# Optimization experiments

Hardware: AMD Instinct MI355X
Metric: run time of the kernel (lower is better)

Reference implementation:

```python
import jax, jax.numpy as jnp
import numpy as np

B, N, HID = 8, 1024, 768
HEADS, LORA, HDIM = 12, 256, 64


def setup_inputs() -> dict:
    key = jax.random.key(0)
    k1, k2, k3 = jax.random.split(key, 3)
    hidden_states = jax.random.normal(k1, (B, N, HID), dtype=jnp.float32)
    attention_mask = jnp.ones((B, N), dtype=jnp.int32)
    # torch Linear weights are [out_features, in_features]
    Wt = jax.random.normal(k2, (HEADS, LORA, HID), dtype=jnp.float32) * (HID ** -0.5)
    Wa = jax.random.normal(k3, (HEADS, HDIM, LORA), dtype=jnp.float32) * (LORA ** -0.5)
    return {"hidden_states": hidden_states, "attention_mask": attention_mask,
            "Wt": Wt, "Wa": Wa}


def reference(hidden_states, attention_mask, Wt, Wa):
    # Per-head LoRA projection, batched over heads instead of a Python loop.
    # t: [b, h, n, head_dim]; repeat(1,1,3) in the original makes q = k = v = t.
    scale = hidden_states.shape[-1] ** -0.5  # input_dim ** -0.5
    t = jnp.einsum('bnd,hld->bhnl', hidden_states, Wt)
    t = jnp.einsum('bhnl,hel->bhne', t, Wa)
    scores = jnp.einsum('bhid,bhjd->bhij', t, t) * scale
    scores = jnp.where(attention_mask[:, None, None, :] == 0, -jnp.inf, scores)
    attn = jax.nn.softmax(scores, axis=-1)
    out = jnp.einsum('bhij,bhjd->bhid', attn, t)  # [b, h, n, d]
    b, h, n, d = out.shape
    return out.transpose(0, 2, 1, 3).reshape(b, n, h * d)
```

## Files before the change

### kernel.cpp

```cpp
#include <hip/hip_runtime.h>
#include <math.h>

#define BATCH 8
#define SEQ   1024
#define HID_  768
#define HEADS 12
#define LORA  256
#define HDIM  64

#define SCALE      0.03608439182435161f
#define SCALE_LOG2 0.05205863235888918f

typedef _Float16 f16_t;
typedef _Float16 f16x4 __attribute__((ext_vector_type(4)));
typedef _Float16 f16x8 __attribute__((ext_vector_type(8)));
typedef float    f32x4 __attribute__((ext_vector_type(4)));
typedef unsigned short ushort_t;

#define GLD16(g, l) __builtin_amdgcn_global_load_lds( \
    (const __attribute__((address_space(1))) void*)(g), \
    (__attribute__((address_space(3))) void*)(l), 16, 0, 0)

#define SW(c, r) ((((c) ^ ((r) & 7)) << 3))

#define N4_HS (BATCH * SEQ * HID_ / 4)
#define N4_WT (HEADS * LORA * HID_ / 4)
#define N4_WA (HEADS * HDIM * LORA / 4)

__global__ __launch_bounds__(256) void cvt_all_kernel(
    const float4* __restrict__ hs, const float4* __restrict__ wt,
    const float4* __restrict__ wa, f16x4* __restrict__ hs_f,
    f16x4* __restrict__ wt_f, f16x4* __restrict__ wa_f)
{
    int stride = gridDim.x * blockDim.x;
    for (int i = blockIdx.x * blockDim.x + threadIdx.x;
         i < N4_HS + N4_WT + N4_WA; i += stride) {
        const float4* s; f16x4* d; int j;
        if (i < N4_HS)                { s = hs; d = hs_f; j = i; }
        else if (i < N4_HS + N4_WT)   { s = wt; d = wt_f; j = i - N4_HS; }
        else                          { s = wa; d = wa_f; j = i - N4_HS - N4_WT; }
        float4 v = s[j];
        f16x4 o = {(f16_t)v.x, (f16_t)v.y, (f16_t)v.z, (f16_t)v.w};
        d[j] = o;
    }
}

__global__ __launch_bounds__(256, 3) void proj_mfma(
    const f16_t* __restrict__ hs_f, const f16_t* __restrict__ wt_f,
    const f16_t* __restrict__ wa_f, f16_t* __restrict__ t_f,
    f16_t* __restrict__ tT_f)
{
    __shared__ __attribute__((aligned(16))) char smem[32768];
    f16_t* s_hs = (f16_t*)smem;
    f16_t* s_wt = (f16_t*)(smem + 16384);
    f16_t* s_t1 = (f16_t*)smem;
    f16_t* s_wa = (f16_t*)(smem + 16384);
    f16_t* s_ob = (f16_t*)smem;

    const int bid   = blockIdx.x;
    const int ntile = bid & 7;
    const int h     = (bid >> 3) % HEADS;
    const int b     = bid / (8 * HEADS);
    const int n0    = ntile * 128;
    const int tid   = threadIdx.x;
    const int w     = tid >> 6;
    const int lane  = tid & 63;
    const int q     = lane >> 4;
    const int mr    = lane & 15;
    const int lrow  = lane >> 3;
    const int gswz  = (((lane & 7) ^ lrow) & 7) * 8;

    const f16_t* hs_g = hs_f + (size_t)b * SEQ * HID_;
    const f16_t* wt_g = wt_f + (size_t)h * LORA * HID_;
    const f16_t* wa_g = wa_f + (size_t)h * HDIM * LORA;

    const f32x4 z4 = {0.f, 0.f, 0.f, 0.f};
    f32x4 accB[2][4];
    #pragma unroll
    for (int mt = 0; mt < 2; ++mt)
        #pragma unroll
        for (int et = 0; et < 4; ++et) accB[mt][et] = z4;

    for (int pass = 0; pass < 2; ++pass) {
        const int lp = pass * 128;

        f32x4 accA[2][8];
        #pragma unroll
        for (int mt = 0; mt < 2; ++mt)
            #pragma unroll
            for (int lt = 0; lt < 8; ++lt) accA[mt][lt] = z4;

        for (int rd = 0; rd < 12; ++rd) {
            const int k0 = rd * 64;
            __syncthreads();
            #pragma unroll
            for (int tt = 0; tt < 4; ++tt) {
                int r0 = w * 32 + tt * 8;
                GLD16(hs_g + (size_t)(n0 + r0 + lrow) * HID_ + k0 + gswz, s_hs + r0 * 64);
            }
            #pragma unroll
            for (int tt = 0; tt < 4; ++tt) {
                int r0 = w * 32 + tt * 8;
                GLD16(wt_g + (size_t)(lp + r0 + lrow) * HID_ + k0 + gswz, s_wt + r0 * 64);
            }
            __syncthreads();

            #pragma unroll
            for (int ks = 0; ks < 2; ++ks) {
                f16x8 a_[2], b_[8];
                #pragma unroll
                for (int mt = 0; mt < 2; ++mt)
                    a_[mt] = *(const f16x8*)(s_hs + (w * 32 + mt * 16 + mr) * 64 + SW(ks * 4 + q, mr));
                #pragma unroll
                for (int lt = 0; lt < 8; ++lt)
                    b_[lt] = *(const f16x8*)(s_wt + (lt * 16 + mr) * 64 + SW(ks * 4 + q, mr));
                #pragma unroll
                for (int mt = 0; mt < 2; ++mt)
                    #pragma unroll
                    for (int lt = 0; lt < 8; ++lt)
                        accA[mt][lt] = __builtin_amdgcn_mfma_f32_16x16x32_f16(a_[mt], b_[lt], accA[mt][lt], 0, 0, 0);
            }
        }

        #pragma unroll
        for (int sub = 0; sub < 2; ++sub) {
            const int l0g = lp + sub * 64;
            __syncthreads();
            #pragma unroll
            for (int mt = 0; mt < 2; ++mt) {
                #pragma unroll
                for (int j = 0; j < 4; ++j) {
                    #pragma unroll
                    for (int r = 0; r < 4; ++r) {
                        int row = w * 32 + mt * 16 + q * 4 + r;
                        int col = j * 16 + mr;
                        s_t1[row * 64 + ((((col >> 3) ^ (row & 7)) << 3) | (col & 7))]
                            = (f16_t)accA[mt][sub * 4 + j][r];
                    }
                }
            }
            #pragma unroll
            for (int tt = 0; tt < 2; ++tt) {
                int r0 = w * 16 + tt * 8;
                GLD16(wa_g + (size_t)(r0 + lrow) * LORA + l0g + gswz, s_wa + r0 * 64);
            }
            __syncthreads();

            #pragma unroll
            for (int ks = 0; ks < 2; ++ks) {
                f16x8 a_[2], b_[4];
                #pragma unroll
                for (int mt = 0; mt < 2; ++mt)
                    a_[mt] = *(const f16x8*)(s_t1 + (w * 32 + mt * 16 + mr) * 64 + SW(ks * 4 + q, mr));
                #pragma unroll
                for (int et = 0; et < 4; ++et)
                    b_[et] = *(const f16x8*)(s_wa + (et * 16 + mr) * 64 + SW(ks * 4 + q, mr));
                #pragma unroll
                for (int mt = 0; mt < 2; ++mt)
                    #pragma unroll
                    for (int et = 0; et < 4; ++et)
                        accB[mt][et] = __builtin_amdgcn_mfma_f32_16x16x32_f16(a_[mt], b_[et], accB[mt][et], 0, 0, 0);
            }
        }
    }

    __syncthreads();
    #pragma unroll
    for (int mt = 0; mt < 2; ++mt) {
        #pragma unroll
        for (int et = 0; et < 4; ++et) {
            #pragma unroll
            for (int r = 0; r < 4; ++r) {
                int row = w * 32 + mt * 16 + q * 4 + r;
                int col = et * 16 + mr;
                s_ob[row * 72 + col] = (f16_t)accB[mt][et][r];
            }
        }
    }
    __syncthreads();

    f16_t* tg = t_f + (((size_t)b * HEADS + h) * SEQ + n0) * HDIM;
    #pragma unroll
    for (int k = 0; k < 4; ++k) {
        int u = tid + k * 256;
        int row = u >> 3, c8 = (u & 7) * 8;
        *(f16x8*)&tg[row * 64 + c8] = *(const f16x8*)&s_ob[row * 72 + c8];
    }
    f16_t* tTg = tT_f + ((size_t)b * HEADS + h) * SEQ * HDIM;
    #pragma unroll
    for (int k = 0; k < 4; ++k) {
        int u = tid + k * 256;
        int e = u & 63, n8 = (u >> 6) * 8;
        f16x8 v;
        #pragma unroll
        for (int j = 0; j < 8; ++j) v[j] = s_ob[(n8 + j) * 72 + e];
        *(f16x8*)&tTg[(size_t)e * SEQ + n0 + n8] = v;
    }
}

__global__ __launch_bounds__(256, 3) void attn_mfma(
    const f16_t* __restrict__ t_f, const f16_t* __restrict__ tT_f,
    const int* __restrict__ mask, float* __restrict__ out)
{
    __shared__ __attribute__((aligned(16))) char smem[34816];
    f16_t* s_k = (f16_t*)smem;
    f16_t* s_v = (f16_t*)(smem + 8192);
    f16_t* s_p = (f16_t*)(smem + 16384);
    float* s_m = (float*)smem;

    const int bid  = blockIdx.x;
    const int it   = bid & 7;
    const int h    = (bid >> 3) % HEADS;
    const int b    = bid / (8 * HEADS);
    const int i0   = it * 128;
    const int tid  = threadIdx.x;
    const int w    = tid >> 6;
    const int lane = tid & 63;
    const int q    = lane >> 4;
    const int mr   = lane & 15;
    const int lrow = lane >> 3;
    const int gswz = (((lane & 7) ^ lrow) & 7) * 8;
    const int ih   = w >> 1;
    const int jh   = w & 1;

    const size_t bh = ((size_t)b * HEADS + h) * SEQ * HDIM;
    const f16_t* th = t_f + bh;
    const f16_t* vh = tT_f + bh;
    const int* mk = mask + (size_t)b * SEQ;

    f16x8 qf[4][2];
    #pragma unroll
    for (int mt = 0; mt < 4; ++mt)
        #pragma unroll
        for (int ks = 0; ks < 2; ++ks) {
            f16x8 v = *(const f16x8*)(th + (size_t)(i0 + ih * 64 + mt * 16 + mr) * 64
                                      + ks * 32 + q * 8);
            #pragma unroll
            for (int j = 0; j < 8; ++j) v[j] = v[j] * (f16_t)SCALE_LOG2;
            qf[mt][ks] = v;
        }

    const f32x4 z4 = {0.f, 0.f, 0.f, 0.f};
    float l_[4] = {0.f, 0.f, 0.f, 0.f};
    f32x4 oT[4][4];
    #pragma unroll
    for (int mt = 0; mt < 4; ++mt)
        #pragma unroll
        for (int et = 0; et < 4; ++et) oT[mt][et] = z4;

    for (int jt6 = 0; jt6 < 16; ++jt6) {
        const int j0 = jt6 * 64;
        __syncthreads();
        #pragma unroll
        for (int t2 = 0; t2 < 2; ++t2) {
            int r0 = w * 16 + t2 * 8;
            GLD16(th + (size_t)(j0 + r0 + lrow) * 64 + gswz,  s_k + r0 * 64);
            GLD16(vh + (size_t)(r0 + lrow) * SEQ + j0 + gswz, s_v + r0 * 64);
        }
        __syncthreads();

        #pragma unroll
        for (int jt = 0; jt < 2; ++jt) {
            f32x4 st[4] = {z4, z4, z4, z4};
            #pragma unroll
            for (int ks = 0; ks < 2; ++ks) {
                f16x8 kf = *(const f16x8*)(s_k + (jh * 32 + jt * 16 + mr) * 64 + SW(ks * 4 + q, mr));
                #pragma unroll
                for (int mt = 0; mt < 4; ++mt)
                    st[mt] = __builtin_amdgcn_mfma_f32_16x16x32_f16(kf, qf[mt][ks], st[mt], 0, 0, 0);
            }
            int4 mv = *(const int4*)(mk + j0 + jh * 32 + jt * 16 + q * 4);
            #pragma unroll
            for (int mt = 0; mt < 4; ++mt) {
                float p0 = (mv.x == 0) ? 0.f : __builtin_amdgcn_exp2f(st[mt][0]);
                float p1 = (mv.y == 0) ? 0.f : __builtin_amdgcn_exp2f(st[mt][1]);
                float p2 = (mv.z == 0) ? 0.f : __builtin_amdgcn_exp2f(st[mt][2]);
                float p3 = (mv.w == 0) ? 0.f : __builtin_amdgcn_exp2f(st[mt][3]);
                l_[mt] += (p0 + p1) + (p2 + p3);
                f16x4 u4 = {(f16_t)p0, (f16_t)p1, (f16_t)p2, (f16_t)p3};
                *(f16x4*)&s_p[(ih * 64 + mt * 16 + mr) * 72 + jh * 32 + jt * 16 + q * 4] = u4;
            }
        }

        f16x8 pf[4];
        #pragma unroll
        for (int mt = 0; mt < 4; ++mt)
            pf[mt] = *(const f16x8*)(s_p + (ih * 64 + mt * 16 + mr) * 72 + jh * 32 + q * 8);
        #pragma unroll
        for (int et = 0; et < 4; ++et) {
            f16x8 vv = *(const f16x8*)(s_v + (et * 16 + mr) * 64 + SW(jh * 4 + q, mr));
            #pragma unroll
            for (int mt = 0; mt < 4; ++mt)
                oT[mt][et] = __builtin_amdgcn_mfma_f32_16x16x32_f16(vv, pf[mt], oT[mt][et], 0, 0, 0);
        }
    }

    #pragma unroll
    for (int mt = 0; mt < 4; ++mt) {
        l_[mt] += __shfl_xor(l_[mt], 16);
        l_[mt] += __shfl_xor(l_[mt], 32);
    }

    __syncthreads();
    if (jh == 1) {
        float* dst = s_m + ((size_t)ih * 64 + lane) * 68;
        #pragma unroll
        for (int mt = 0; mt < 4; ++mt) {
            #pragma unroll
            for (int et = 0; et < 4; ++et)
                *(f32x4*)&dst[(mt * 4 + et) * 4] = oT[mt][et];
            dst[64 + mt] = l_[mt];
        }
    }
    __syncthreads();
    if (jh == 0) {
        const float* src = s_m + ((size_t)ih * 64 + lane) * 68;
        #pragma unroll
        for (int mt = 0; mt < 4; ++mt) {
            float lt = l_[mt] + src[64 + mt];
            float inv = (lt > 0.f) ? 1.f / lt : 0.f;
            int n = i0 + ih * 64 + mt * 16 + mr;
            #pragma unroll
            for (int et = 0; et < 4; ++et) {
                f32x4 o2 = *(const f32x4*)&src[(mt * 4 + et) * 4];
                float4 v = {(oT[mt][et][0] + o2[0]) * inv, (oT[mt][et][1] + o2[1]) * inv,
                            (oT[mt][et][2] + o2[2]) * inv, (oT[mt][et][3] + o2[3]) * inv};
                *(float4*)&out[((size_t)b * SEQ + n) * (HEADS * HDIM) + h * HDIM + et * 16 + q * 4] = v;
            }
        }
    }
}

extern "C" void kernel_launch(void* const* d_in, const int* in_sizes, int n_in,
                              void* d_out, int out_size, void* d_ws, size_t ws_size,
                              hipStream_t stream) {
    const float* hs   = (const float*)d_in[0];
    const int*   mask = (const int*)d_in[1];
    const float* Wt   = (const float*)d_in[2];
    const float* Wa   = (const float*)d_in[3];
    float* out = (float*)d_out;

    char* ws = (char*)d_ws;
    f16_t* t_f  = (f16_t*)ws;
    f16_t* tT_f = (f16_t*)(ws + 12582912);
    f16_t* hs_f = (f16_t*)(ws + 25165824);
    f16_t* wt_f = (f16_t*)(ws + 37748736);
    f16_t* wa_f = (f16_t*)(ws + 42467328);

    cvt_all_kernel<<<1024, 256, 0, stream>>>(
        (const float4*)hs, (const float4*)Wt, (const float4*)Wa,
        (f16x4*)hs_f, (f16x4*)wt_f, (f16x4*)wa_f);

    proj_mfma<<<BATCH * HEADS * (SEQ / 128), 256, 0, stream>>>(
        hs_f, wt_f, wa_f, t_f, tT_f);

    attn_mfma<<<BATCH * HEADS * (SEQ / 128), 256, 0, stream>>>(
        t_f, tT_f, mask, out);
}
```

Measured before the change: 180.0 us.

## Precombine per-head Wa·Wt into one weight, replacing two-stage projection GEMM

Adds a small fp32 kernel that multiplies Wa by Wt per head, producing a fused 64x768 fp16 weight. The projection then becomes a single GEMM of hidden states against that weight, instead of first projecting to the 256-wide LoRA space and then down to 64. This cuts the projection FLOPs by roughly 5x and drops the fp16 conversion of Wt and Wa. The new GEMM loads operands straight from global memory without LDS staging, which may give less efficient memory access, and the rounding order differs slightly from the reference.

```diff
diff --git a/kernel.cpp b/kernel.cpp
--- a/kernel.cpp
+++ b/kernel.cpp
@@ -12,10 +12,10 @@
 #define SCALE_LOG2 0.05205863235888918f
 
 typedef _Float16 f16_t;
+typedef _Float16 f16x2 __attribute__((ext_vector_type(2)));
 typedef _Float16 f16x4 __attribute__((ext_vector_type(4)));
 typedef _Float16 f16x8 __attribute__((ext_vector_type(8)));
 typedef float    f32x4 __attribute__((ext_vector_type(4)));
-typedef unsigned short ushort_t;
 
 #define GLD16(g, l) __builtin_amdgcn_global_load_lds( \
     (const __attribute__((address_space(1))) void*)(g), \
@@ -24,38 +24,83 @@
 #define SW(c, r) ((((c) ^ ((r) & 7)) << 3))
 
 #define N4_HS (BATCH * SEQ * HID_ / 4)
-#define N4_WT (HEADS * LORA * HID_ / 4)
-#define N4_WA (HEADS * HDIM * LORA / 4)
-
-__global__ __launch_bounds__(256) void cvt_all_kernel(
-    const float4* __restrict__ hs, const float4* __restrict__ wt,
-    const float4* __restrict__ wa, f16x4* __restrict__ hs_f,
-    f16x4* __restrict__ wt_f, f16x4* __restrict__ wa_f)
+
+__global__ __launch_bounds__(256) void cvt_hs_kernel(
+    const float4* __restrict__ hs, f16x4* __restrict__ hs_f)
 {
     int stride = gridDim.x * blockDim.x;
-    for (int i = blockIdx.x * blockDim.x + threadIdx.x;
-         i < N4_HS + N4_WT + N4_WA; i += stride) {
-        const float4* s; f16x4* d; int j;
-        if (i < N4_HS)                { s = hs; d = hs_f; j = i; }
-        else if (i < N4_HS + N4_WT)   { s = wt; d = wt_f; j = i - N4_HS; }
-        else                          { s = wa; d = wa_f; j = i - N4_HS - N4_WT; }
-        float4 v = s[j];
+    for (int i = blockIdx.x * blockDim.x + threadIdx.x; i < N4_HS; i += stride) {
+        float4 v = hs[i];
         f16x4 o = {(f16_t)v.x, (f16_t)v.y, (f16_t)v.z, (f16_t)v.w};
-        d[j] = o;
-    }
-}
-
-__global__ __launch_bounds__(256, 3) void proj_mfma(
-    const f16_t* __restrict__ hs_f, const f16_t* __restrict__ wt_f,
-    const f16_t* __restrict__ wa_f, f16_t* __restrict__ t_f,
-    f16_t* __restrict__ tT_f)
+        hs_f[i] = o;
+    }
+}
+
+__global__ __launch_bounds__(256) void fuse_w_kernel(
+    const float* __restrict__ Wt, const float* __restrict__ Wa,
+    f16_t* __restrict__ w_f)
 {
-    __shared__ __attribute__((aligned(16))) char smem[32768];
-    f16_t* s_hs = (f16_t*)smem;
-    f16_t* s_wt = (f16_t*)(smem + 16384);
-    f16_t* s_t1 = (f16_t*)smem;
-    f16_t* s_wa = (f16_t*)(smem + 16384);
-    f16_t* s_ob = (f16_t*)smem;
+    __shared__ float s_a[64][68];
+    __shared__ float s_b[64][36];
+
+    const int bid = blockIdx.x;
+    const int h   = bid / 24;
+    const int d0  = (bid % 24) * 32;
+    const int tid = threadIdx.x;
+    const int ty  = tid >> 4;
+    const int tx  = tid & 15;
+
+    const float* wa_g = Wa + (size_t)h * HDIM * LORA;
+    const float* wt_g = Wt + (size_t)h * LORA * HID_;
+
+    float acc[4][2] = {{0.f, 0.f}, {0.f, 0.f}, {0.f, 0.f}, {0.f, 0.f}};
+
+    for (int kc = 0; kc < 4; ++kc) {
+        const int l0 = kc * 64;
+        if (kc) __syncthreads();
+        #pragma unroll
+        for (int k = 0; k < 4; ++k) {
+            int u = tid + k * 256;
+            int r = u >> 4, c4 = (u & 15) * 4;
+            *(float4*)&s_a[r][c4] = *(const float4*)&wa_g[(size_t)r * LORA + l0 + c4];
+        }
+        #pragma unroll
+        for (int k = 0; k < 2; ++k) {
+            int u = tid + k * 256;
+            int r = u >> 3, c4 = (u & 7) * 4;
+            *(float4*)&s_b[r][c4] = *(const float4*)&wt_g[(size_t)(l0 + r) * HID_ + d0 + c4];
+        }
+        __syncthreads();
+
+        #pragma unroll 8
+        for (int l = 0; l < 64; ++l) {
+            float a0 = s_a[ty * 4 + 0][l];
+            float a1 = s_a[ty * 4 + 1][l];
+            float a2 = s_a[ty * 4 + 2][l];
+            float a3 = s_a[ty * 4 + 3][l];
+            float b0 = s_b[l][tx * 2 + 0];
+            float b1 = s_b[l][tx * 2 + 1];
+            acc[0][0] = fmaf(a0, b0, acc[0][0]); acc[0][1] = fmaf(a0, b1, acc[0][1]);
+            acc[1][0] = fmaf(a1, b0, acc[1][0]); acc[1][1] = fmaf(a1, b1, acc[1][1]);
+            acc[2][0] = fmaf(a2, b0, acc[2][0]); acc[2][1] = fmaf(a2, b1, acc[2][1]);
+            acc[3][0] = fmaf(a3, b0, acc[3][0]); acc[3][1] = fmaf(a3, b1, acc[3][1]);
+        }
+    }
+
+    f16_t* wg = w_f + (size_t)h * HDIM * HID_;
+    #pragma unroll
+    for (int i = 0; i < 4; ++i) {
+        int e = ty * 4 + i;
+        f16x2 o = {(f16_t)acc[i][0], (f16_t)acc[i][1]};
+        *(f16x2*)&wg[(size_t)e * HID_ + d0 + tx * 2] = o;
+    }
+}
+
+__global__ __launch_bounds__(256, 3) void gemm_t(
+    const f16_t* __restrict__ hs_f, const f16_t* __restrict__ w_f,
+    f16_t* __restrict__ t_f, f16_t* __restrict__ tT_f)
+{
+    __shared__ __attribute__((aligned(16))) f16_t s_ob[128 * 72];
 
     const int bid   = blockIdx.x;
     const int ntile = bid & 7;
@@ -67,104 +112,33 @@
     const int lane  = tid & 63;
     const int q     = lane >> 4;
     const int mr    = lane & 15;
-    const int lrow  = lane >> 3;
-    const int gswz  = (((lane & 7) ^ lrow) & 7) * 8;
-
-    const f16_t* hs_g = hs_f + (size_t)b * SEQ * HID_;
-    const f16_t* wt_g = wt_f + (size_t)h * LORA * HID_;
-    const f16_t* wa_g = wa_f + (size_t)h * HDIM * LORA;
+
+    const f16_t* ag = hs_f + ((size_t)b * SEQ + n0 + w * 32 + mr) * HID_ + q * 8;
+    const f16_t* bg = w_f + ((size_t)h * HDIM + mr) * HID_ + q * 8;
 
     const f32x4 z4 = {0.f, 0.f, 0.f, 0.f};
-    f32x4 accB[2][4];
+    f32x4 acc[2][4];
     #pragma unroll
     for (int mt = 0; mt < 2; ++mt)
         #pragma unroll
-        for (int et = 0; et < 4; ++et) accB[mt][et] = z4;
-
-    for (int pass = 0; pass < 2; ++pass) {
-        const int lp = pass * 128;
-
-        f32x4 accA[2][8];
+        for (int et = 0; et < 4; ++et) acc[mt][et] = z4;
+
+    #pragma unroll
+    for (int kc = 0; kc < 24; ++kc) {
+        f16x8 a_[2], b_[4];
         #pragma unroll
         for (int mt = 0; mt < 2; ++mt)
-            #pragma unroll
-            for (int lt = 0; lt < 8; ++lt) accA[mt][lt] = z4;
-
-        for (int rd = 0; rd < 12; ++rd) {
-            const int k0 = rd * 64;
-            __syncthreads();
-            #pragma unroll
-            for (int tt = 0; tt < 4; ++tt) {
-                int r0 = w * 32 + tt * 8;
-                GLD16(hs_g + (size_t)(n0 + r0 + lrow) * HID_ + k0 + gswz, s_hs + r0 * 64);
-            }
-            #pragma unroll
-            for (int tt = 0; tt < 4; ++tt) {
-                int r0 = w * 32 + tt * 8;
-                GLD16(wt_g + (size_t)(lp + r0 + lrow) * HID_ + k0 + gswz, s_wt + r0 * 64);
-            }
-            __syncthreads();
-
-            #pragma unroll
-            for (int ks = 0; ks < 2; ++ks) {
-                f16x8 a_[2], b_[8];
-                #pragma unroll
-                for (int mt = 0; mt < 2; ++mt)
-                    a_[mt] = *(const f16x8*)(s_hs + (w * 32 + mt * 16 + mr) * 64 + SW(ks * 4 + q, mr));
-                #pragma unroll
-                for (int lt = 0; lt < 8; ++lt)
-                    b_[lt] = *(const f16x8*)(s_wt + (lt * 16 + mr) * 64 + SW(ks * 4 + q, mr));
-                #pragma unroll
-                for (int mt = 0; mt < 2; ++mt)
-                    #pragma unroll
-                    for (int lt = 0; lt < 8; ++lt)
-                        accA[mt][lt] = __builtin_amdgcn_mfma_f32_16x16x32_f16(a_[mt], b_[lt], accA[mt][lt], 0, 0, 0);
-            }
-        }
-
-        #pragma unroll
-        for (int sub = 0; sub < 2; ++sub) {
-            const int l0g = lp + sub * 64;
-            __syncthreads();
-            #pragma unroll
-            for (int mt = 0; mt < 2; ++mt) {
-                #pragma unroll
-                for (int j = 0; j < 4; ++j) {
-                    #pragma unroll
-                    for (int r = 0; r < 4; ++r) {
-                        int row = w * 32 + mt * 16 + q * 4 + r;
-                        int col = j * 16 + mr;
-                        s_t1[row * 64 + ((((col >> 3) ^ (row & 7)) << 3) | (col & 7))]
-                            = (f16_t)accA[mt][sub * 4 + j][r];
-                    }
-                }
-            }
-            #pragma unroll
-            for (int tt = 0; tt < 2; ++tt) {
-                int r0 = w * 16 + tt * 8;
-                GLD16(wa_g + (size_t)(r0 + lrow) * LORA + l0g + gswz, s_wa + r0 * 64);
-            }
-            __syncthreads();
-
-            #pragma unroll
-            for (int ks = 0; ks < 2; ++ks) {
-                f16x8 a_[2], b_[4];
-                #pragma unroll
-                for (int mt = 0; mt < 2; ++mt)
-                    a_[mt] = *(const f16x8*)(s_t1 + (w * 32 + mt * 16 + mr) * 64 + SW(ks * 4 + q, mr));
-                #pragma unroll
-                for (int et = 0; et < 4; ++et)
-                    b_[et] = *(const f16x8*)(s_wa + (et * 16 + mr) * 64 + SW(ks * 4 + q, mr));
-                #pragma unroll
-                for (int mt = 0; mt < 2; ++mt)
-                    #pragma unroll
-                    for (int et = 0; et < 4; ++et)
-                        accB[mt][et] = __builtin_amdgcn_mfma_f32_16x16x32_f16(a_[mt], b_[et], accB[mt][et], 0, 0, 0);
-            }
-        }
-    }
-
-    __syncthreads();
+            a_[mt] = *(const f16x8*)(ag + (size_t)mt * 16 * HID_ + kc * 32);
+        #pragma unroll
+        for (int et = 0; et < 4; ++et)
+            b_[et] = *(const f16x8*)(bg + (size_t)et * 16 * HID_ + kc * 32);
+        #pragma unroll
+        for (int mt = 0; mt < 2; ++mt)
+            #pragma unroll
+            for (int et = 0; et < 4; ++et)
+                acc[mt][et] = __builtin_amdgcn_mfma_f32_16x16x32_f16(a_[mt], b_[et], acc[mt][et], 0, 0, 0);
+    }
+
     #pragma unroll
     for (int mt = 0; mt < 2; ++mt) {
         #pragma unroll
@@ -173,7 +147,7 @@
             for (int r = 0; r < 4; ++r) {
                 int row = w * 32 + mt * 16 + q * 4 + r;
                 int col = et * 16 + mr;
-                s_ob[row * 72 + col] = (f16_t)accB[mt][et][r];
+                s_ob[row * 72 + col] = (f16_t)acc[mt][et][r];
             }
         }
     }
@@ -344,15 +318,13 @@
     f16_t* t_f  = (f16_t*)ws;
     f16_t* tT_f = (f16_t*)(ws + 12582912);
     f16_t* hs_f = (f16_t*)(ws + 25165824);
-    f16_t* wt_f = (f16_t*)(ws + 37748736);
-    f16_t* wa_f = (f16_t*)(ws + 42467328);
-
-    cvt_all_kernel<<<1024, 256, 0, stream>>>(
-        (const float4*)hs, (const float4*)Wt, (const float4*)Wa,
-        (f16x4*)hs_f, (f16x4*)wt_f, (f16x4*)wa_f);
-
-    proj_mfma<<<BATCH * HEADS * (SEQ / 128), 256, 0, stream>>>(
-        hs_f, wt_f, wa_f, t_f, tT_f);
+    f16_t* w_f  = (f16_t*)(ws + 37748736);
+
+    cvt_hs_kernel<<<1024, 256, 0, stream>>>((const float4*)hs, (f16x4*)hs_f);
+
+    fuse_w_kernel<<<HEADS * (HID_ / 32), 256, 0, stream>>>(Wt, Wa, w_f);
+
+    gemm_t<<<BATCH * HEADS * (SEQ / 128), 256, 0, stream>>>(hs_f, w_f, t_f, tT_f);
 
     attn_mfma<<<BATCH * HEADS * (SEQ / 128), 256, 0, stream>>>(
         t_f, tT_f, mask, out);
```

Result: slower. 192.6 us (+7.0%).
